# Optimization experiments

Hardware: AMD Instinct MI355X
Metric: run time of the kernel (lower is better)

## Reference

```python
import jax, jax.numpy as jnp
import numpy as np

HEAD_DIM = 256
N_HEADS = 8
ROPE_BASE = 10000.0
EPS = 1e-6


def _rms(x):
    xf = x.astype(jnp.float32)
    return xf * jax.lax.rsqrt(jnp.mean(xf * xf, axis=-1, keepdims=True) + EPS)


def _rotate_half(x):
    x1, x2 = jnp.split(x, 2, axis=-1)
    return jnp.concatenate([-x2, x1], axis=-1)


def _mlp(h, wg, wu, wd):
    # Gemma gated MLP with gelu_pytorch_tanh activation
    return (jax.nn.gelu(h @ wg, approximate=True) * (h @ wu)) @ wd


def _qkv(h, wq, wk, wv):
    B, S, _ = h.shape
    q = (h @ wq).reshape(B, S, N_HEADS, HEAD_DIM).transpose(0, 2, 1, 3)  # [B,H,S,Dh]
    k = (h @ wk).reshape(B, S, HEAD_DIM)                                  # MQA: 1 kv head
    v = (h @ wv).reshape(B, S, HEAD_DIM)
    return q, k, v


def _forward(x_prefix, x_expert, attention_mask, adarms_cond, position_ids,
             p_ln1, p_wq, p_wk, p_wv, p_wo, p_ln2, p_wgate, p_wup, p_wdown,
             e_ada1_w, e_ada1_b, e_wq, e_wk, e_wv, e_wo, e_ada2_w, e_ada2_b,
             e_wgate, e_wup, e_wdown):
    B, S1, Dp = x_prefix.shape
    S2 = x_expert.shape[1]

    # --- pre-attention norms: plain Gemma RMSNorm (prefix), AdaRMS (expert) ---
    h_p = _rms(x_prefix) * (1.0 + p_ln1)
    mod1 = adarms_cond @ e_ada1_w + e_ada1_b                  # [B, 3*De]
    sc1, sh1, g1 = jnp.split(mod1, 3, axis=-1)
    h_e = _rms(x_expert) * (1.0 + sc1[:, None]) + sh1[:, None]
    gate1_e = g1[:, None]                                      # [B,1,De]

    # --- concatenated QKV across the two streams ---
    q_p, k_p, v_p = _qkv(h_p, p_wq, p_wk, p_wv)
    q_e, k_e, v_e = _qkv(h_e, e_wq, e_wk, e_wv)
    q = jnp.concatenate([q_p, q_e], axis=2)                    # [B,H,S,Dh]
    k = jnp.concatenate([k_p, k_e], axis=1)                    # [B,S,Dh]
    v = jnp.concatenate([v_p, v_e], axis=1)

    # --- rotary embedding on joint positions ---
    inv_freq = 1.0 / (ROPE_BASE ** (jnp.arange(0, HEAD_DIM, 2, dtype=jnp.float32) / HEAD_DIM))
    ang = position_ids.astype(jnp.float32)[..., None] * inv_freq
    emb = jnp.concatenate([ang, ang], axis=-1)                 # [B,S,Dh]
    cos, sin = jnp.cos(emb), jnp.sin(emb)
    q = q * cos[:, None] + _rotate_half(q) * sin[:, None]
    k = k * cos + _rotate_half(k) * sin

    # --- eager MQA attention ---
    scaling = HEAD_DIM ** -0.5
    scores = jnp.einsum('bhqd,bkd->bhqk', q, k) * scaling + attention_mask
    probs = jax.nn.softmax(scores.astype(jnp.float32), axis=-1)
    att = jnp.einsum('bhqk,bkd->bhqd', probs, v)
    att = att.transpose(0, 2, 1, 3).reshape(B, S1 + S2, N_HEADS * HEAD_DIM)

    # --- prefix stream: o_proj, residual, RMSNorm, gated MLP, residual ---
    res_p = x_prefix + att[:, :S1] @ p_wo
    h2_p = _rms(res_p) * (1.0 + p_ln2)
    out_p = res_p + _mlp(h2_p, p_wgate, p_wup, p_wdown)

    # --- expert stream: gated residuals from AdaRMS ---
    res_e = x_expert + gate1_e * (att[:, S1:] @ e_wo)
    mod2 = adarms_cond @ e_ada2_w + e_ada2_b
    sc2, sh2, g2 = jnp.split(mod2, 3, axis=-1)
    h2_e = _rms(res_e) * (1.0 + sc2[:, None]) + sh2[:, None]
    out_e = res_e + g2[:, None] * _mlp(h2_e, e_wgate, e_wup, e_wdown)
    return out_p, out_e


def setup_inputs() -> dict:
    key = jax.random.key(0)
    ks = iter(jax.random.split(key, 32))
    B, S1, S2 = 4, 768, 64
    Dp, De, Dh, H = 2048, 1024, 256, 8
    Fp, Fe = 16384, 4096

    def w(shape, s=0.02):
        return jax.random.normal(next(ks), shape, dtype=jnp.float32) * s

    return dict(
        x_prefix=jax.random.normal(next(ks), (B, S1, Dp), dtype=jnp.float32),
        x_expert=jax.random.normal(next(ks), (B, S2, De), dtype=jnp.float32),
        attention_mask=jnp.zeros((B, 1, S1 + S2, S1 + S2), dtype=jnp.float32),
        adarms_cond=jax.random.normal(next(ks), (B, De), dtype=jnp.float32),
        position_ids=jnp.sort(jax.random.randint(next(ks), (B, S1 + S2), 0, S1 + S2), axis=-1),
        p_ln1=jnp.zeros((Dp,), jnp.float32),
        p_wq=w((Dp, H * Dh)), p_wk=w((Dp, Dh)), p_wv=w((Dp, Dh)), p_wo=w((H * Dh, Dp)),
        p_ln2=jnp.zeros((Dp,), jnp.float32),
        p_wgate=w((Dp, Fp)), p_wup=w((Dp, Fp)), p_wdown=w((Fp, Dp)),
        e_ada1_w=w((De, 3 * De)), e_ada1_b=jnp.zeros((3 * De,), jnp.float32),
        e_wq=w((De, H * Dh)), e_wk=w((De, Dh)), e_wv=w((De, Dh)), e_wo=w((H * Dh, De)),
        e_ada2_w=w((De, 3 * De)), e_ada2_b=jnp.zeros((3 * De,), jnp.float32),
        e_wgate=w((De, Fe)), e_wup=w((De, Fe)), e_wdown=w((Fe, De)),
    )


def reference(x_prefix, x_expert, attention_mask, adarms_cond, position_ids,
              p_ln1, p_wq, p_wk, p_wv, p_wo, p_ln2, p_wgate, p_wup, p_wdown,
              e_ada1_w, e_ada1_b, e_wq, e_wk, e_wv, e_wo, e_ada2_w, e_ada2_b,
              e_wgate, e_wup, e_wdown):
    return _forward(x_prefix, x_expert, attention_mask, adarms_cond, position_ids,
                    p_ln1, p_wq, p_wk, p_wv, p_wo, p_ln2, p_wgate, p_wup, p_wdown,
                    e_ada1_w, e_ada1_b, e_wq, e_wk, e_wv, e_wo, e_ada2_w, e_ada2_b,
                    e_wgate, e_wup, e_wdown)
```

## Files before the change

kernel.cpp:

```cpp
#include <hip/hip_runtime.h>
#include <stdint.h>

typedef unsigned short ushort_t;
typedef __attribute__((ext_vector_type(8))) short short8;
typedef __attribute__((ext_vector_type(4))) float f32x4;

#define DEVINL __device__ __forceinline__

DEVINL ushort_t f2bf(float f){
  union { float f; uint32_t u; } v; v.f = f;
  uint32_t u = v.u;
  uint32_t r = (u + 0x7fffu + ((u >> 16) & 1u)) >> 16;
  return (ushort_t)r;
}
DEVINL float bf2f(ushort_t h){
  union { uint32_t u; float f; } v; v.u = ((uint32_t)h) << 16;
  return v.f;
}
DEVINL f32x4 mfma16(short8 a, short8 b, f32x4 c){
  return __builtin_amdgcn_mfma_f32_16x16x32_bf16(a, b, c, 0, 0, 0);
}
DEVINL void gload_lds16(const void* g, void* l){
  __builtin_amdgcn_global_load_lds((const __attribute__((address_space(1))) void*)g,
                                   (__attribute__((address_space(3))) void*)l, 16, 0, 0);
}
DEVINL float gelu_tanh(float x){
  return 0.5f * x * (1.f + tanhf(0.7978845608028654f * (x + 0.044715f * x * x * x)));
}

__global__ void transpose_bf16(const float* __restrict__ W, ushort_t* __restrict__ Wt,
                               int K, int N)
{
  __shared__ ushort_t tile[64 * 65];
  const int t = threadIdx.x;
  const int k0 = blockIdx.y * 64, n0 = blockIdx.x * 64;
#pragma unroll
  for (int rr = 0; rr < 4; ++rr){
    const int row = rr * 16 + (t >> 4);
    const int c4 = (t & 15) * 4;
    float4 v = *(const float4*)&W[(size_t)(k0 + row) * N + n0 + c4];
    ushort_t* dst = &tile[row * 65 + c4];
    dst[0] = f2bf(v.x); dst[1] = f2bf(v.y); dst[2] = f2bf(v.z); dst[3] = f2bf(v.w);
  }
  __syncthreads();
  const int n = t >> 2, kc = (t & 3) * 16;
  __align__(16) ushort_t tmp[16];
#pragma unroll
  for (int j = 0; j < 16; ++j) tmp[j] = tile[(kc + j) * 65 + n];
  ushort_t* out = &Wt[(size_t)(n0 + n) * K + k0 + kc];
  *(short8*)&out[0] = *(short8*)&tmp[0];
  *(short8*)&out[8] = *(short8*)&tmp[8];
}

__global__ void mod_kernel(const float* __restrict__ cond,
                           const float* __restrict__ w1, const float* __restrict__ b1,
                           const float* __restrict__ w2, const float* __restrict__ b2,
                           float* __restrict__ mod1, float* __restrict__ mod2)
{
  __shared__ float cs[1024];
  const int bid = blockIdx.x, tid = threadIdx.x;
  const int which = bid / 48, rem = bid % 48, b = rem / 12, j0 = (rem % 12) * 256;
  const float* W = which ? w2 : w1;
  const float* bias = which ? b2 : b1;
  float* out = which ? mod2 : mod1;
#pragma unroll
  for (int i = 0; i < 4; ++i) cs[i * 256 + tid] = cond[b * 1024 + i * 256 + tid];
  __syncthreads();
  const int j = j0 + tid;
  float acc = bias[j];
  for (int k = 0; k < 1024; ++k) acc = fmaf(cs[k], W[(size_t)k * 3072 + j], acc);
  out[b * 3072 + j] = acc;
}

__global__ void rms_kernel(const float* __restrict__ x, ushort_t* __restrict__ out, int D,
                           const float* __restrict__ sw, const float* __restrict__ sh,
                           int mod_rpb, int mod_stride)
{
  const int row = blockIdx.x, tid = threadIdx.x;
  const float* xr = x + (size_t)row * D;
  const int nc = D >> 10;
  float ss = 0.f;
  for (int c = 0; c < nc; ++c){
    float4 v = *(const float4*)&xr[c * 1024 + tid * 4];
    ss += v.x * v.x + v.y * v.y + v.z * v.z + v.w * v.w;
  }
  for (int o = 32; o > 0; o >>= 1) ss += __shfl_xor(ss, o);
  __shared__ float red[4];
  if ((tid & 63) == 0) red[tid >> 6] = ss;
  __syncthreads();
  const float scale = rsqrtf((red[0] + red[1] + red[2] + red[3]) / (float)D + 1e-6f);
  const float* swp = sw;
  const float* shp = sh;
  if (mod_rpb){
    int bb = row / mod_rpb;
    swp += (size_t)bb * mod_stride;
    if (shp) shp += (size_t)bb * mod_stride;
  }
  for (int c = 0; c < nc; ++c){
    const int d = c * 1024 + tid * 4;
    float4 v = *(const float4*)&xr[d];
    float vv[4] = {v.x, v.y, v.z, v.w};
#pragma unroll
    for (int i = 0; i < 4; ++i){
      float tv = vv[i] * scale * (1.f + swp[d + i]);
      if (shp) tv += shp[d + i];
      out[(size_t)row * D + d + i] = f2bf(tv);
    }
  }
}

__global__ void rope_kernel(const ushort_t* __restrict__ qkv_p, const ushort_t* __restrict__ qkv_e,
                            const int* __restrict__ pos_ids,
                            ushort_t* __restrict__ q_all, ushort_t* __restrict__ k_all,
                            ushort_t* __restrict__ vT)
{
  const int tok = blockIdx.x, tid = threadIdx.x;
  int b, s;
  const ushort_t* src;
  if (tok < 3072){ b = tok / 768; s = tok - b * 768; src = qkv_p + (size_t)tok * 2560; }
  else { int te = tok - 3072; b = te >> 6; s = 768 + (te & 63); src = qkv_e + (size_t)te * 2560; }
  const int pos = pos_ids[b * 832 + s];
  __shared__ float cs[128], sn[128];
  if (tid < 128){
    float f = powf(10000.f, -(float)tid * (1.f / 128.f));
    float a = (float)pos * f;
    cs[tid] = cosf(a); sn[tid] = sinf(a);
  }
  __syncthreads();
#pragma unroll
  for (int c = 0; c < 10; ++c){
    const int n = c * 256 + tid;
    const float v = bf2f(src[n]);
    if (n < 2048){
      const int h = n >> 8, d = n & 255;
      const float o = bf2f(src[(h << 8) + ((d < 128) ? (d + 128) : (d - 128))]);
      const int dd = d & 127;
      const float r = (d < 128) ? v * cs[dd] - o * sn[dd] : v * cs[dd] + o * sn[dd];
      q_all[(((size_t)(b * 8 + h)) * 832 + s) * 256 + d] = f2bf(r);
    } else if (n < 2304){
      const int d = n - 2048;
      const float o = bf2f(src[2048 + ((d < 128) ? (d + 128) : (d - 128))]);
      const int dd = d & 127;
      const float r = (d < 128) ? v * cs[dd] - o * sn[dd] : v * cs[dd] + o * sn[dd];
      k_all[((size_t)(b * 832) + s) * 256 + d] = f2bf(r);
    } else {
      const int d = n - 2304;
      vT[((size_t)(b * 256) + d) * 832 + s] = src[n];
    }
  }
}

__global__ void __launch_bounds__(256, 2)
attn_kernel(const ushort_t* __restrict__ q_all, const ushort_t* __restrict__ k_all,
            const ushort_t* __restrict__ vT, const float* __restrict__ mask,
            ushort_t* __restrict__ att)
{
  __shared__ __align__(16) ushort_t Ks[64 * 256];
  __shared__ __align__(16) ushort_t Vs[256 * 64];
  __shared__ __align__(16) ushort_t Ps[4][16 * 72];
  const int tid = threadIdx.x, lane = tid & 63, wid = tid >> 6;
  const int l15 = lane & 15, lg = lane >> 4;
  const int qt = blockIdx.x, h = blockIdx.y, b = blockIdx.z;
  const int q0 = qt * 64 + wid * 16;

  short8 qf[8];
  {
    const ushort_t* qr = q_all + (((size_t)(b * 8 + h) * 832) + q0 + l15) * 256;
#pragma unroll
    for (int s = 0; s < 8; ++s) qf[s] = *(const short8*)&qr[s * 32 + lg * 8];
  }

  f32x4 accO[16] = {};
  float mrow[4] = {-3.0e38f, -3.0e38f, -3.0e38f, -3.0e38f};
  float lrow[4] = {0.f, 0.f, 0.f, 0.f};

  for (int kt = 0; kt < 13; ++kt){
    const int s0 = kt * 64;
#pragma unroll
    for (int i = 0; i < 8; ++i){
      const int o = i * 256 + tid;
      gload_lds16(k_all + ((size_t)(b * 832) + s0 + (o >> 5)) * 256 + (o & 31) * 8, &Ks[o * 8]);
      gload_lds16(vT + ((size_t)(b * 256) + (o >> 3)) * 832 + s0 + (o & 7) * 8, &Vs[o * 8]);
    }
    __syncthreads();

    f32x4 sc[4] = {};
#pragma unroll
    for (int s = 0; s < 8; ++s){
#pragma unroll
      for (int nf = 0; nf < 4; ++nf){
        short8 kb = *(const short8*)&Ks[(nf * 16 + l15) * 256 + s * 32 + lg * 8];
        sc[nf] = mfma16(qf[s], kb, sc[nf]);
      }
    }
#pragma unroll
    for (int nf = 0; nf < 4; ++nf){
#pragma unroll
      for (int r = 0; r < 4; ++r){
        const int q = q0 + lg * 4 + r;
        const int kk = s0 + nf * 16 + l15;
        sc[nf][r] = sc[nf][r] * 0.0625f + mask[((size_t)b * 832 + q) * 832 + kk];
      }
    }
    float al[4];
#pragma unroll
    for (int r = 0; r < 4; ++r){
      float tm = fmaxf(fmaxf(sc[0][r], sc[1][r]), fmaxf(sc[2][r], sc[3][r]));
      tm = fmaxf(tm, __shfl_xor(tm, 1));
      tm = fmaxf(tm, __shfl_xor(tm, 2));
      tm = fmaxf(tm, __shfl_xor(tm, 4));
      tm = fmaxf(tm, __shfl_xor(tm, 8));
      const float mnew = fmaxf(mrow[r], tm);
      al[r] = __expf(mrow[r] - mnew);
      mrow[r] = mnew;
      float rs = 0.f;
#pragma unroll
      for (int nf = 0; nf < 4; ++nf){
        const float p = __expf(sc[nf][r] - mnew);
        rs += p;
        Ps[wid][(lg * 4 + r) * 72 + nf * 16 + l15] = f2bf(p);
      }
      rs += __shfl_xor(rs, 1);
      rs += __shfl_xor(rs, 2);
      rs += __shfl_xor(rs, 4);
      rs += __shfl_xor(rs, 8);
      lrow[r] = lrow[r] * al[r] + rs;
    }
#pragma unroll
    for (int nd = 0; nd < 16; ++nd){
#pragma unroll
      for (int r = 0; r < 4; ++r) accO[nd][r] *= al[r];
    }
#pragma unroll
    for (int ks = 0; ks < 2; ++ks){
      short8 pa = *(const short8*)&Ps[wid][l15 * 72 + ks * 32 + lg * 8];
#pragma unroll
      for (int nd = 0; nd < 16; ++nd){
        short8 vb = *(const short8*)&Vs[(nd * 16 + l15) * 64 + ks * 32 + lg * 8];
        accO[nd] = mfma16(pa, vb, accO[nd]);
      }
    }
    __syncthreads();
  }
#pragma unroll
  for (int nd = 0; nd < 16; ++nd){
#pragma unroll
    for (int r = 0; r < 4; ++r){
      const int q = q0 + lg * 4 + r;
      const int d = nd * 16 + l15;
      att[((size_t)(b * 832) + q) * 2048 + h * 256 + d] = f2bf(accO[nd][r] / lrow[r]);
    }
  }
}

template<int EPI>
__global__ void __launch_bounds__(256, 2)
gemm_bt(const ushort_t* __restrict__ A, int lda, int a_rpb, int a_bstride, int a_r0,
        const ushort_t* __restrict__ Bt, int ldb,
        void* __restrict__ Cv, int N, int K,
        const void* __restrict__ Xv,
        const float* __restrict__ gatep, int gate_stride, int gate_rpb,
        size_t pstride)
{
  __shared__ __align__(16) ushort_t As[128 * 64];
  __shared__ __align__(16) ushort_t Bs[128 * 64];
  const int tid = threadIdx.x;
  const int lane = tid & 63;
  const int l15 = lane & 15, lg = lane >> 4;
  const int wid = tid >> 6;
  const int wm = (wid >> 1) * 64, wn = (wid & 1) * 64;
  const int m0 = blockIdx.y * 128, n0 = blockIdx.x * 128;
  const int z = blockIdx.z;
  const int kbeg = z * K, kend = z * K + K;

  size_t abase[4], bbase[4];
  const int k8 = (tid & 7) * 8;
#pragma unroll
  for (int i = 0; i < 4; ++i){
    const int row = (i * 256 + tid) >> 3;
    const int r = m0 + row;
    const int bb = r / a_rpb;
    const int arow = bb * a_bstride + a_r0 + (r - bb * a_rpb);
    abase[i] = (size_t)arow * lda + k8;
    bbase[i] = (size_t)(n0 + row) * ldb + k8;
  }

  f32x4 acc[4][4] = {};

  for (int kt = kbeg; kt < kend; kt += 64){
#pragma unroll
    for (int i = 0; i < 4; ++i){
      gload_lds16(A + abase[i] + kt, &As[(i * 256 + tid) * 8]);
      gload_lds16(Bt + bbase[i] + kt, &Bs[(i * 256 + tid) * 8]);
    }
    __syncthreads();
#pragma unroll
    for (int s = 0; s < 2; ++s){
      const int ko = s * 32 + lg * 8;
      short8 af[4], bfr[4];
#pragma unroll
      for (int i = 0; i < 4; ++i) af[i] = *(const short8*)&As[(wm + i * 16 + l15) * 64 + ko];
#pragma unroll
      for (int j = 0; j < 4; ++j) bfr[j] = *(const short8*)&Bs[(wn + j * 16 + l15) * 64 + ko];
#pragma unroll
      for (int i = 0; i < 4; ++i)
#pragma unroll
        for (int j = 0; j < 4; ++j)
          acc[i][j] = mfma16(af[i], bfr[j], acc[i][j]);
    }
    __syncthreads();
  }

#pragma unroll
  for (int i = 0; i < 4; ++i){
#pragma unroll
    for (int r = 0; r < 4; ++r){
      const int m = m0 + wm + i * 16 + lg * 4 + r;
#pragma unroll
      for (int j = 0; j < 4; ++j){
        const int n = n0 + wn + j * 16 + l15;
        const size_t idx = (size_t)m * N + n;
        const float v = acc[i][j][r];
        if (EPI == 0){
          ((ushort_t*)Cv)[idx] = f2bf(v);
        } else if (EPI == 1){
          const float g = bf2f(((const ushort_t*)Xv)[idx]);
          ((ushort_t*)Cv)[idx] = f2bf(gelu_tanh(g) * v);
        } else if (EPI == 2){
          ((float*)Cv)[idx] = ((const float*)Xv)[idx] + v;
        } else if (EPI == 3){
          const int bb = m / gate_rpb;
          ((float*)Cv)[idx] = ((const float*)Xv)[idx] + gatep[(size_t)bb * gate_stride + n] * v;
        } else {
          ((float*)Cv)[(size_t)z * pstride + idx] = v;
        }
      }
    }
  }
}

__global__ void reduce4(const float* __restrict__ part, const float* __restrict__ res,
                        float* __restrict__ out, int total4, size_t pstride)
{
  int i = blockIdx.x * blockDim.x + threadIdx.x;
  const int stride = gridDim.x * blockDim.x;
  for (; i < total4; i += stride){
    const size_t e = (size_t)i * 4;
    float4 a = *(const float4*)&res[e];
#pragma unroll
    for (int z = 0; z < 4; ++z){
      float4 p = *(const float4*)&part[(size_t)z * pstride + e];
      a.x += p.x; a.y += p.y; a.z += p.z; a.w += p.w;
    }
    *(float4*)&out[e] = a;
  }
}

__global__ void fuse_gelu(const float* __restrict__ pg, const float* __restrict__ pu,
                          ushort_t* __restrict__ out, int total4, size_t pstride)
{
  int i = blockIdx.x * blockDim.x + threadIdx.x;
  const int stride = gridDim.x * blockDim.x;
  for (; i < total4; i += stride){
    const size_t e = (size_t)i * 4;
    float4 g = *(const float4*)&pg[e];
    float4 u = *(const float4*)&pu[e];
#pragma unroll
    for (int z = 1; z < 4; ++z){
      float4 a = *(const float4*)&pg[(size_t)z * pstride + e];
      float4 b = *(const float4*)&pu[(size_t)z * pstride + e];
      g.x += a.x; g.y += a.y; g.z += a.z; g.w += a.w;
      u.x += b.x; u.y += b.y; u.z += b.z; u.w += b.w;
    }
    out[e + 0] = f2bf(gelu_tanh(g.x) * u.x);
    out[e + 1] = f2bf(gelu_tanh(g.y) * u.y);
    out[e + 2] = f2bf(gelu_tanh(g.z) * u.z);
    out[e + 3] = f2bf(gelu_tanh(g.w) * u.w);
  }
}

__global__ void reduce_gated(const float* __restrict__ part, size_t pstride, int nz,
                             const float* __restrict__ base, const float* __restrict__ gate,
                             int gstride, int rpb, int N,
                             float* __restrict__ out, int total4)
{
  int i = blockIdx.x * blockDim.x + threadIdx.x;
  const int stride = gridDim.x * blockDim.x;
  for (; i < total4; i += stride){
    const size_t e = (size_t)i * 4;
    const int row = (int)(e / N), n = (int)(e % N);
    const int b = row / rpb;
    float4 s = *(const float4*)&part[e];
    for (int z = 1; z < nz; ++z){
      float4 p = *(const float4*)&part[(size_t)z * pstride + e];
      s.x += p.x; s.y += p.y; s.z += p.z; s.w += p.w;
    }
    float4 bs = *(const float4*)&base[e];
    const float* gp = &gate[(size_t)b * gstride + n];
    bs.x += gp[0] * s.x; bs.y += gp[1] * s.y; bs.z += gp[2] * s.z; bs.w += gp[3] * s.w;
    *(float4*)&out[e] = bs;
  }
}

extern "C" void kernel_launch(void* const* d_in, const int* in_sizes, int n_in,
                              void* d_out, int out_size, void* d_ws, size_t ws_size,
                              hipStream_t stream)
{
  const float* x_prefix = (const float*)d_in[0];
  const float* x_expert = (const float*)d_in[1];
  const float* mask     = (const float*)d_in[2];
  const float* cond     = (const float*)d_in[3];
  const int*   pos      = (const int*)d_in[4];
  const float* p_ln1    = (const float*)d_in[5];
  const float* p_wq     = (const float*)d_in[6];
  const float* p_wk     = (const float*)d_in[7];
  const float* p_wv     = (const float*)d_in[8];
  const float* p_wo     = (const float*)d_in[9];
  const float* p_ln2    = (const float*)d_in[10];
  const float* p_wgate  = (const float*)d_in[11];
  const float* p_wup    = (const float*)d_in[12];
  const float* p_wdown  = (const float*)d_in[13];
  const float* e_ada1_w = (const float*)d_in[14];
  const float* e_ada1_b = (const float*)d_in[15];
  const float* e_wq     = (const float*)d_in[16];
  const float* e_wk     = (const float*)d_in[17];
  const float* e_wv     = (const float*)d_in[18];
  const float* e_wo     = (const float*)d_in[19];
  const float* e_ada2_w = (const float*)d_in[20];
  const float* e_ada2_b = (const float*)d_in[21];
  const float* e_wgate  = (const float*)d_in[22];
  const float* e_wup    = (const float*)d_in[23];
  const float* e_wdown  = (const float*)d_in[24];

  char* ws = (char*)d_ws;
  size_t off = 0;
  auto alloc = [&](size_t bytes) -> char* {
    char* p = ws + off;
    off += bytes;
    off = (off + 255) & ~(size_t)255;
    return p;
  };

  ushort_t* t_wqkv_p  = (ushort_t*)alloc((size_t)2560 * 2048 * 2);
  ushort_t* t_wo_p    = (ushort_t*)alloc((size_t)2048 * 2048 * 2);
  ushort_t* t_wgate_p = (ushort_t*)alloc((size_t)16384 * 2048 * 2);
  ushort_t* t_wup_p   = (ushort_t*)alloc((size_t)16384 * 2048 * 2);
  ushort_t* t_wdown_p = (ushort_t*)alloc((size_t)2048 * 16384 * 2);
  ushort_t* t_wqkv_e  = (ushort_t*)alloc((size_t)2560 * 1024 * 2);
  ushort_t* t_wo_e    = (ushort_t*)alloc((size_t)1024 * 2048 * 2);
  ushort_t* t_wgate_e = (ushort_t*)alloc((size_t)4096 * 1024 * 2);
  ushort_t* t_wup_e   = (ushort_t*)alloc((size_t)4096 * 1024 * 2);
  ushort_t* t_wdown_e = (ushort_t*)alloc((size_t)1024 * 4096 * 2);
  float* mod1 = (float*)alloc((size_t)4 * 3072 * 4);
  float* mod2 = (float*)alloc((size_t)4 * 3072 * 4);
  float* res_p = (float*)alloc((size_t)3072 * 2048 * 4);
  float* res_e = (float*)alloc((size_t)256 * 1024 * 4);
  ushort_t* h2_p = (ushort_t*)alloc((size_t)3072 * 2048 * 2);
  ushort_t* h2_e = (ushort_t*)alloc((size_t)256 * 1024 * 2);
  ushort_t* g_e  = (ushort_t*)alloc((size_t)256 * 4096 * 2);

  const size_t zone_off = off;
  ushort_t* h_p   = (ushort_t*)alloc((size_t)3072 * 2048 * 2);
  ushort_t* h_e   = (ushort_t*)alloc((size_t)256 * 1024 * 2);
  ushort_t* qkv_p = (ushort_t*)alloc((size_t)3072 * 2560 * 2);
  ushort_t* qkv_e = (ushort_t*)alloc((size_t)256 * 2560 * 2);
  ushort_t* q_all = (ushort_t*)alloc((size_t)4 * 8 * 832 * 256 * 2);
  ushort_t* k_all = (ushort_t*)alloc((size_t)4 * 832 * 256 * 2);
  ushort_t* vTb   = (ushort_t*)alloc((size_t)4 * 256 * 832 * 2);
  ushort_t* att   = (ushort_t*)alloc((size_t)4 * 832 * 2048 * 2);
  const size_t phase1_end = off;
  ushort_t* g_p = (ushort_t*)(ws + zone_off);

  float* partials = (float*)t_wgate_p;
  const size_t PSTRIDE_P = (size_t)3072 * 2048;
  float* pwo = (float*)(ws + zone_off);
  const size_t PSTRIDE_E = (size_t)256 * 1024;
  float* pg = (float*)t_wgate_p;
  float* pu = pg + (size_t)4 * 256 * 4096;
  float* pd = pu + (size_t)4 * 256 * 4096;
  const size_t PSTRIDE_GE = (size_t)256 * 4096;

  const size_t g_p_end = zone_off + (size_t)3072 * 16384 * 2;
  const size_t needed = (phase1_end > g_p_end) ? phase1_end : g_p_end;
  if (ws_size < needed) return;

  const int BIG = 1 << 30;

  transpose_bf16<<<dim3(2048/64, 2048/64), 256, 0, stream>>>(p_wq, t_wqkv_p, 2048, 2048);
  transpose_bf16<<<dim3(256/64, 2048/64), 256, 0, stream>>>(p_wk, t_wqkv_p + (size_t)2048*2048, 2048, 256);
  transpose_bf16<<<dim3(256/64, 2048/64), 256, 0, stream>>>(p_wv, t_wqkv_p + (size_t)2304*2048, 2048, 256);
  transpose_bf16<<<dim3(2048/64, 2048/64), 256, 0, stream>>>(p_wo, t_wo_p, 2048, 2048);
  transpose_bf16<<<dim3(16384/64, 2048/64), 256, 0, stream>>>(p_wgate, t_wgate_p, 2048, 16384);
  transpose_bf16<<<dim3(16384/64, 2048/64), 256, 0, stream>>>(p_wup, t_wup_p, 2048, 16384);
  transpose_bf16<<<dim3(2048/64, 16384/64), 256, 0, stream>>>(p_wdown, t_wdown_p, 16384, 2048);
  transpose_bf16<<<dim3(2048/64, 1024/64), 256, 0, stream>>>(e_wq, t_wqkv_e, 1024, 2048);
  transpose_bf16<<<dim3(256/64, 1024/64), 256, 0, stream>>>(e_wk, t_wqkv_e + (size_t)2048*1024, 1024, 256);
  transpose_bf16<<<dim3(256/64, 1024/64), 256, 0, stream>>>(e_wv, t_wqkv_e + (size_t)2304*1024, 1024, 256);
  transpose_bf16<<<dim3(1024/64, 2048/64), 256, 0, stream>>>(e_wo, t_wo_e, 2048, 1024);
  transpose_bf16<<<dim3(4096/64, 1024/64), 256, 0, stream>>>(e_wgate, t_wgate_e, 1024, 4096);
  transpose_bf16<<<dim3(4096/64, 1024/64), 256, 0, stream>>>(e_wup, t_wup_e, 1024, 4096);
  transpose_bf16<<<dim3(1024/64, 4096/64), 256, 0, stream>>>(e_wdown, t_wdown_e, 4096, 1024);

  mod_kernel<<<96, 256, 0, stream>>>(cond, e_ada1_w, e_ada1_b, e_ada2_w, e_ada2_b, mod1, mod2);

  rms_kernel<<<3072, 256, 0, stream>>>(x_prefix, h_p, 2048, p_ln1, nullptr, 0, 0);
  rms_kernel<<<256, 256, 0, stream>>>(x_expert, h_e, 1024, mod1, mod1 + 1024, 64, 3072);

  gemm_bt<0><<<dim3(20, 24), 256, 0, stream>>>(h_p, 2048, BIG, 0, 0, t_wqkv_p, 2048,
                                               qkv_p, 2560, 2048, nullptr, nullptr, 0, 1, 0);
  gemm_bt<0><<<dim3(20, 2), 256, 0, stream>>>(h_e, 1024, BIG, 0, 0, t_wqkv_e, 1024,
                                              qkv_e, 2560, 1024, nullptr, nullptr, 0, 1, 0);

  rope_kernel<<<3328, 256, 0, stream>>>(qkv_p, qkv_e, pos, q_all, k_all, vTb);

  attn_kernel<<<dim3(13, 8, 4), 256, 0, stream>>>(q_all, k_all, vTb, mask, att);

  gemm_bt<2><<<dim3(16, 24), 256, 0, stream>>>(att, 2048, 768, 832, 0, t_wo_p, 2048,
                                               res_p, 2048, 2048, x_prefix, nullptr, 0, 1, 0);
  gemm_bt<4><<<dim3(8, 2, 4), 256, 0, stream>>>(att, 2048, 64, 832, 768, t_wo_e, 2048,
                                                pwo, 1024, 512, nullptr, nullptr, 0, 1, PSTRIDE_E);
  reduce_gated<<<256, 256, 0, stream>>>(pwo, PSTRIDE_E, 4, x_expert, mod1 + 2048, 3072, 64, 1024,
                                        res_e, (256 * 1024) / 4);

  rms_kernel<<<3072, 256, 0, stream>>>(res_p, h2_p, 2048, p_ln2, nullptr, 0, 0);
  rms_kernel<<<256, 256, 0, stream>>>(res_e, h2_e, 1024, mod2, mod2 + 1024, 64, 3072);

  gemm_bt<0><<<dim3(128, 24), 256, 0, stream>>>(h2_p, 2048, BIG, 0, 0, t_wgate_p, 2048,
                                                g_p, 16384, 2048, nullptr, nullptr, 0, 1, 0);
  gemm_bt<1><<<dim3(128, 24), 256, 0, stream>>>(h2_p, 2048, BIG, 0, 0, t_wup_p, 2048,
                                                g_p, 16384, 2048, g_p, nullptr, 0, 1, 0);
  gemm_bt<4><<<dim3(16, 24, 4), 256, 0, stream>>>(g_p, 16384, BIG, 0, 0, t_wdown_p, 16384,
                                                  partials, 2048, 4096, nullptr, nullptr, 0, 1, PSTRIDE_P);
  reduce4<<<2048, 256, 0, stream>>>(partials, res_p, (float*)d_out,
                                    (3072 * 2048) / 4, PSTRIDE_P);

  gemm_bt<4><<<dim3(32, 2, 4), 256, 0, stream>>>(h2_e, 1024, BIG, 0, 0, t_wgate_e, 1024,
                                                 pg, 4096, 256, nullptr, nullptr, 0, 1, PSTRIDE_GE);
  gemm_bt<4><<<dim3(32, 2, 4), 256, 0, stream>>>(h2_e, 1024, BIG, 0, 0, t_wup_e, 1024,
                                                 pu, 4096, 256, nullptr, nullptr, 0, 1, PSTRIDE_GE);
  fuse_gelu<<<1024, 256, 0, stream>>>(pg, pu, g_e, (256 * 4096) / 4, PSTRIDE_GE);
  gemm_bt<4><<<dim3(8, 2, 8), 256, 0, stream>>>(g_e, 4096, BIG, 0, 0, t_wdown_e, 4096,
                                                pd, 1024, 512, nullptr, nullptr, 0, 1, PSTRIDE_E);
  reduce_gated<<<256, 256, 0, stream>>>(pd, PSTRIDE_E, 8, res_e, mod2 + 2048, 3072, 64, 1024,
                                        (float*)d_out + (size_t)3072 * 2048, (256 * 1024) / 4);
}
```

Measured before the change: 1.336 ms.

## Add 256x256-tile 8-wave GEMM with pipelined LDS staging for prefix MLP

```diff
diff --git a/kernel.cpp b/kernel.cpp
--- a/kernel.cpp
+++ b/kernel.cpp
@@ -27,6 +27,13 @@
 DEVINL float gelu_tanh(float x){
   return 0.5f * x * (1.f + tanhf(0.7978845608028654f * (x + 0.044715f * x * x * x)));
 }
+
+#define BAR() __builtin_amdgcn_s_barrier()
+#define LGK0() asm volatile("s_waitcnt lgkmcnt(0)" ::: "memory")
+#define VMC4() asm volatile("s_waitcnt vmcnt(4)" ::: "memory")
+#define VMC0() asm volatile("s_waitcnt vmcnt(0)" ::: "memory")
+#define PRIO1() __builtin_amdgcn_s_setprio(1)
+#define PRIO0() __builtin_amdgcn_s_setprio(0)
 
 __global__ void transpose_bf16(const float* __restrict__ W, ushort_t* __restrict__ Wt,
                                int K, int N)
@@ -331,6 +338,120 @@
         } else if (EPI == 3){
           const int bb = m / gate_rpb;
           ((float*)Cv)[idx] = ((const float*)Xv)[idx] + gatep[(size_t)bb * gate_stride + n] * v;
+        } else {
+          ((float*)Cv)[(size_t)z * pstride + idx] = v;
+        }
+      }
+    }
+  }
+}
+
+#define MMAQ(AF, BF, MQ, NQ) \
+  { _Pragma("unroll") for (int i_ = 0; i_ < 4; ++i_){ \
+      _Pragma("unroll") for (int j_ = 0; j_ < 2; ++j_){ \
+        _Pragma("unroll") for (int s_ = 0; s_ < 2; ++s_){ \
+          acc[(MQ)*4 + i_][(NQ)*2 + j_] = \
+            mfma16(AF[i_][s_], BF[j_][s_], acc[(MQ)*4 + i_][(NQ)*2 + j_]); } } } }
+
+template<int EPI>
+__global__ void __launch_bounds__(512, 1)
+gemm8(const ushort_t* __restrict__ A, int lda,
+      const ushort_t* __restrict__ Bt, int ldb,
+      void* __restrict__ Cv, int N, int klen,
+      const void* __restrict__ Xv, size_t pstride)
+{
+  __shared__ __align__(16) ushort_t As[2][256 * 64];
+  __shared__ __align__(16) ushort_t Bs[2][256 * 64];
+
+  const int tid = threadIdx.x;
+  const int lane = tid & 63, wid = tid >> 6;
+  const int l15 = lane & 15, lg = lane >> 4;
+  const int wm = (wid >> 2) * 128, wn = (wid & 3) * 64;
+
+  const int gx = gridDim.x, nwg = gx * gridDim.y;
+  const int orig = blockIdx.y * gx + blockIdx.x;
+  const int q = nwg >> 3, r = nwg & 7;
+  const int xcd = orig & 7, lo = orig >> 3;
+  const int wg = (xcd < r ? xcd * (q + 1) : r * (q + 1) + (xcd - r) * q) + lo;
+  const int m0 = (wg / gx) * 256, n0 = (wg % gx) * 256;
+  const int z = blockIdx.z;
+  const size_t k0 = (size_t)z * klen;
+  const int NT = klen >> 6;
+
+  auto stage = [&](int buf, int half, int kt){
+    const ushort_t* src; int ld, r0; ushort_t* dst;
+    if (half < 2){ src = A;  ld = lda; r0 = m0 + half * 128; dst = &As[buf][half * 8192]; }
+    else         { src = Bt; ld = ldb; r0 = n0 + (half - 2) * 128; dst = &Bs[buf][(half - 2) * 8192]; }
+#pragma unroll
+    for (int c = 0; c < 2; ++c){
+      const int idx = c * 512 + tid;
+      const int row = idx >> 3, slot = idx & 7;
+      gload_lds16(src + (size_t)(r0 + row) * ld + k0 + kt + ((slot ^ (row & 7)) << 3),
+                  dst + idx * 8);
+    }
+  };
+  auto readA = [&](short8 (&f)[4][2], int buf, int mq){
+#pragma unroll
+    for (int i = 0; i < 4; ++i){
+      const int row = wm + mq * 64 + i * 16 + l15;
+#pragma unroll
+      for (int s = 0; s < 2; ++s)
+        f[i][s] = *(const short8*)&As[buf][row * 64 + (((s * 4 + lg) ^ (row & 7)) << 3)];
+    }
+  };
+  auto readB = [&](short8 (&f)[2][2], int buf, int nq){
+#pragma unroll
+    for (int j = 0; j < 2; ++j){
+      const int row = wn + nq * 32 + j * 16 + l15;
+#pragma unroll
+      for (int s = 0; s < 2; ++s)
+        f[j][s] = *(const short8*)&Bs[buf][row * 64 + (((s * 4 + lg) ^ (row & 7)) << 3)];
+    }
+  };
+
+  stage(0, 0, 0); stage(0, 1, 0); stage(0, 2, 0); stage(0, 3, 0);
+  if (NT > 1){ stage(1, 2, 64); stage(1, 0, 64); VMC4(); } else { VMC0(); }
+  BAR();
+
+  short8 af[4][2], bq0[2][2], bq1[2][2];
+  f32x4 acc[8][4] = {};
+
+  for (int t = 0; t < NT; ++t){
+    const int cur = t & 1, nxt = cur ^ 1;
+    const int kc1 = (t + 1) << 6, kc2 = (t + 2) << 6;
+    readA(af, cur, 0);
+    readB(bq0, cur, 0);
+    if (t + 1 < NT) stage(nxt, 1, kc1);
+    BAR(); LGK0();
+    PRIO1(); MMAQ(af, bq0, 0, 0); PRIO0(); BAR();
+    readB(bq1, cur, 1);
+    if (t + 1 < NT) stage(nxt, 3, kc1);
+    BAR(); LGK0();
+    PRIO1(); MMAQ(af, bq1, 0, 1); PRIO0(); BAR();
+    readA(af, cur, 1);
+    if (t + 2 < NT) stage(cur, 2, kc2);
+    BAR(); LGK0();
+    PRIO1(); MMAQ(af, bq1, 1, 1); PRIO0(); BAR();
+    if (t + 2 < NT){ stage(cur, 0, kc2); VMC4(); } else { VMC0(); }
+    BAR();
+    PRIO1(); MMAQ(af, bq0, 1, 0); PRIO0(); BAR();
+  }
+
+#pragma unroll
+  for (int i = 0; i < 8; ++i){
+#pragma unroll
+    for (int rr = 0; rr < 4; ++rr){
+      const int m = m0 + wm + i * 16 + lg * 4 + rr;
+#pragma unroll
+      for (int j = 0; j < 4; ++j){
+        const int n = n0 + wn + j * 16 + l15;
+        const size_t idx = (size_t)m * N + n;
+        const float v = acc[i][j][rr];
+        if (EPI == 0){
+          ((ushort_t*)Cv)[idx] = f2bf(v);
+        } else if (EPI == 1){
+          const float g = bf2f(((const ushort_t*)Xv)[idx]);
+          ((ushort_t*)Cv)[idx] = f2bf(gelu_tanh(g) * v);
         } else {
           ((float*)Cv)[(size_t)z * pstride + idx] = v;
         }
@@ -525,12 +646,12 @@
   rms_kernel<<<3072, 256, 0, stream>>>(res_p, h2_p, 2048, p_ln2, nullptr, 0, 0);
   rms_kernel<<<256, 256, 0, stream>>>(res_e, h2_e, 1024, mod2, mod2 + 1024, 64, 3072);
 
-  gemm_bt<0><<<dim3(128, 24), 256, 0, stream>>>(h2_p, 2048, BIG, 0, 0, t_wgate_p, 2048,
-                                                g_p, 16384, 2048, nullptr, nullptr, 0, 1, 0);
-  gemm_bt<1><<<dim3(128, 24), 256, 0, stream>>>(h2_p, 2048, BIG, 0, 0, t_wup_p, 2048,
-                                                g_p, 16384, 2048, g_p, nullptr, 0, 1, 0);
-  gemm_bt<4><<<dim3(16, 24, 4), 256, 0, stream>>>(g_p, 16384, BIG, 0, 0, t_wdown_p, 16384,
-                                                  partials, 2048, 4096, nullptr, nullptr, 0, 1, PSTRIDE_P);
+  gemm8<0><<<dim3(64, 12, 1), 512, 0, stream>>>(h2_p, 2048, t_wgate_p, 2048,
+                                                g_p, 16384, 2048, nullptr, 0);
+  gemm8<1><<<dim3(64, 12, 1), 512, 0, stream>>>(h2_p, 2048, t_wup_p, 2048,
+                                                g_p, 16384, 2048, g_p, 0);
+  gemm8<4><<<dim3(8, 12, 4), 512, 0, stream>>>(g_p, 16384, t_wdown_p, 16384,
+                                               partials, 2048, 4096, nullptr, PSTRIDE_P);
   reduce4<<<2048, 256, 0, stream>>>(partials, res_p, (float*)d_out,
                                     (3072 * 2048) / 4, PSTRIDE_P);
 
```

Result: slower. 1.393 ms (+4.3%).
